# Kernel tuning notes

Hardware: AMD Instinct MI355X
Metric: run time of the kernel (lower is better)

## Reference

```python
import jax, jax.numpy as jnp
import numpy as np

EMBED, HEADS, LEVELS, POINTS, CAMS, ZANCH = 256, 8, 4, 8, 6, 4
HEAD_DIM = EMBED // HEADS
NQ, BS = 10000, 1
SHAPES = np.array([[92, 160], [46, 80], [23, 40], [12, 20]], dtype=np.int64)
NV = int((SHAPES[:, 0] * SHAPES[:, 1]).sum())  # 19560


def setup_inputs() -> dict:
    key = jax.random.key(0)
    ks = jax.random.split(key, 10)
    f = lambda k, s, sc=1.0: jax.random.normal(k, s, dtype=jnp.float32) * sc
    lsi = np.concatenate([[0], np.cumsum(SHAPES[:, 0] * SHAPES[:, 1])[:-1]]).astype(np.int64)
    return dict(
        query=f(ks[0], (BS, NQ, EMBED)),
        query_pos=f(ks[1], (BS, NQ, EMBED)),
        value=f(ks[2], (CAMS, NV, BS, EMBED)),
        reference_points=jax.random.uniform(ks[3], (CAMS, BS, NQ, ZANCH, 2), dtype=jnp.float32),
        bev_mask=jax.random.bernoulli(ks[4], 0.3, (CAMS, BS, NQ, ZANCH)),
        spatial_shapes=jnp.asarray(SHAPES),
        level_start_index=jnp.asarray(lsi),
        Wv=f(ks[5], (EMBED, EMBED), 0.02), bv=jnp.zeros((EMBED,), jnp.float32),
        Woff=f(ks[6], (EMBED, HEADS * LEVELS * POINTS * 2), 0.02),
        boff=f(ks[7], (HEADS * LEVELS * POINTS * 2,), 0.5),
        Watt=f(ks[8], (EMBED, HEADS * LEVELS * POINTS), 0.02),
        batt=jnp.zeros((HEADS * LEVELS * POINTS,), jnp.float32),
        Wout=f(ks[9], (EMBED, EMBED), 0.02), bout=jnp.zeros((EMBED,), jnp.float32),
    )


def _bilinear_gather(v2, x, y, H, W):
    # v2: (BH, H*W, hd); x, y: (BH, N) pixel coords. grid_sample bilinear,
    # align_corners=False, padding_mode='zeros' semantics.
    x0 = jnp.floor(x); y0 = jnp.floor(y)
    lx = x - x0; ly = y - y0
    x0i = x0.astype(jnp.int32); y0i = y0.astype(jnp.int32)
    out = jnp.zeros(x.shape + (v2.shape[-1],), v2.dtype)
    for dx, dy, w in ((0, 0, (1 - lx) * (1 - ly)), (1, 0, lx * (1 - ly)),
                      (0, 1, (1 - lx) * ly), (1, 1, lx * ly)):
        xi = x0i + dx; yi = y0i + dy
        valid = (xi >= 0) & (xi < W) & (yi >= 0) & (yi < H)
        idx = jnp.clip(yi, 0, H - 1) * W + jnp.clip(xi, 0, W - 1)
        g = jnp.take_along_axis(v2, idx[..., None], axis=1)
        out = out + g * (w * valid.astype(v2.dtype))[..., None]
    return out


def _ms_deform_attn(q, v, ref, shapes, lsi, Wv, bv, Woff, boff, Watt, batt):
    # q: (B, nq, C); v: (B, nv, C); ref: (B, nq, D, 2)
    B, nq, C = q.shape
    v = (v @ Wv + bv).reshape(B, -1, HEADS, HEAD_DIM)
    off = (q @ Woff + boff).reshape(B, nq, HEADS, LEVELS, POINTS, 2)
    attw = jax.nn.softmax((q @ Watt + batt).reshape(B, nq, HEADS, LEVELS * POINTS), axis=-1)
    attw = attw.reshape(B, nq, HEADS, LEVELS, POINTS)
    # offset normalizer: (w_l, h_l) per level
    norm = jnp.asarray(np.stack([shapes[:, 1], shapes[:, 0]], -1), q.dtype)  # (L, 2)
    off = off / norm[None, None, None, :, None, :]
    off = off.reshape(B, nq, HEADS, LEVELS, POINTS // ZANCH, ZANCH, 2)
    loc = (ref[:, :, None, None, None] + off).reshape(B, nq, HEADS, LEVELS, POINTS, 2)
    acc = jnp.zeros((B, HEADS, nq, HEAD_DIM), q.dtype)
    for l in range(LEVELS):
        H, W = int(shapes[l, 0]), int(shapes[l, 1])
        s = int(lsi[l])
        vl = v[:, s:s + H * W].transpose(0, 2, 1, 3).reshape(B * HEADS, H * W, HEAD_DIM)
        ll = loc[:, :, :, l].transpose(0, 2, 1, 3, 4).reshape(B * HEADS, nq * POINTS, 2)
        x = ll[..., 0] * W - 0.5
        y = ll[..., 1] * H - 0.5
        samp = _bilinear_gather(vl, x, y, H, W).reshape(B, HEADS, nq, POINTS, HEAD_DIM)
        w = attw[:, :, :, l].transpose(0, 2, 1, 3)  # (B, HEADS, nq, POINTS)
        acc = acc + (samp * w[..., None]).sum(3)
    return acc.transpose(0, 2, 1, 3).reshape(B, nq, C)


def reference(query, query_pos, value, reference_points, bev_mask, spatial_shapes,
              level_start_index, Wv, bv, Woff, boff, Watt, batt, Wout, bout):
    shapes = np.asarray(spatial_shapes)
    lsi = np.asarray(level_start_index)
    B, nq, C = query.shape
    cams = value.shape[0]
    q = query + query_pos
    # replicate queries per camera (equivalent to rebatch-by-mask: unselected
    # outputs are masked out before accumulation)
    q_cam = jnp.broadcast_to(q[:, None], (B, cams, nq, C)).reshape(B * cams, nq, C)
    v = value.transpose(2, 0, 1, 3).reshape(B * cams, -1, C)
    ref = reference_points.transpose(1, 0, 2, 3, 4).reshape(B * cams, nq, ZANCH, 2)
    out = _ms_deform_attn(q_cam, v, ref, shapes, lsi, Wv, bv, Woff, boff, Watt, batt)
    out = out.reshape(B, cams, nq, C)
    # query selection per camera uses batch 0 of bev_mask, as in the original
    m = (bev_mask[:, 0].sum(-1) > 0)  # (cams, nq)
    slots = (out * m[None, :, :, None].astype(out.dtype)).sum(1)  # (B, nq, C)
    count = (bev_mask.sum(-1) > 0).astype(query.dtype).transpose(1, 2, 0).sum(-1)
    count = jnp.maximum(count, 1.0)  # (B, nq)
    slots = slots / count[..., None]
    # dropout in eval mode is identity
    return slots @ Wout + bout + query
```

## Files before the change

### kernel.cpp

```cpp
#include <hip/hip_runtime.h>
#include <hip/hip_bf16.h>

constexpr int NQ = 10000, NV = 19560, CAMS = 6, EMBED = 256, HEADS = 8,
              HEAD_DIM = 32, LEVELS = 4, POINTS = 8;
constexpr int MQ_PAD = 10112;
constexpr int MV_PAD = 117376;

typedef unsigned int u32;
typedef unsigned short u16;
typedef unsigned char u8;
typedef __attribute__((ext_vector_type(8))) short short8v;
typedef __attribute__((ext_vector_type(4))) float f32x4;
typedef __attribute__((ext_vector_type(2))) float f32x2;

__device__ inline u16 f2bf(float f) {
  __hip_bfloat16 b = __float2bfloat16(f);
  return *(u16*)&b;
}

__global__ void conv_bf16_kernel(const float* __restrict__ a, const float* __restrict__ b,
                                 u16* __restrict__ dst, int M, int Mpad) {
  int i = blockIdx.x * blockDim.x + threadIdx.x;
  if (i >= Mpad * 32) return;
  int row = i >> 5;
  int col = (i & 31) * 8;
  u16 o[8];
  if (row < M) {
    const float* pa = a + (size_t)row * 256 + col;
#pragma unroll
    for (int j = 0; j < 8; ++j) {
      float v = pa[j];
      if (b) v += b[(size_t)row * 256 + col + j];
      o[j] = f2bf(v);
    }
  } else {
#pragma unroll
    for (int j = 0; j < 8; ++j) o[j] = 0;
  }
  *(short8v*)&dst[(size_t)row * 256 + col] = *(short8v*)o;
}

__global__ void transpose_w_kernel(const float* __restrict__ src, u16* __restrict__ dst, int N) {
  int g = blockIdx.x * blockDim.x + threadIdx.x;
  if (g >= N * 256) return;
  int n = g >> 8, k = g & 255;
  dst[(size_t)n * 256 + k] = f2bf(src[(size_t)k * N + n]);
}

__global__ void mask_kernel(const int* __restrict__ bev, unsigned char* __restrict__ m,
                            float* __restrict__ cinv) {
  int q = blockIdx.x * blockDim.x + threadIdx.x;
  if (q >= NQ) return;
  int cnt = 0;
  for (int c = 0; c < CAMS; ++c) {
    int any = 0;
    for (int z = 0; z < 4; ++z) any |= bev[((size_t)c * NQ + q) * 4 + z];
    m[c * NQ + q] = (unsigned char)(any != 0);
    cnt += (any != 0);
  }
  cinv[q] = 1.0f / (float)(cnt > 0 ? cnt : 1);
}

__global__ __launch_bounds__(256) void gemm_mfma(
    const u16* __restrict__ A, const u16* __restrict__ Bt,
    const float* __restrict__ bias, const float* __restrict__ add,
    void* __restrict__ Cout, int M, int N, int mode) {
  constexpr int K = 256, BK = 64;
  __shared__ u16 As[128 * BK];
  __shared__ u16 Bs[128 * BK];
  const int tid = threadIdx.x;
  const int lane = tid & 63, w = tid >> 6;
  const int wr = w >> 1, wc = w & 1;
  const int row0 = blockIdx.y * 128, col0 = blockIdx.x * 128;
  f32x4 acc[4][4] = {};

  for (int k0 = 0; k0 < K; k0 += BK) {
    short8v areg[4], breg[4];
#pragma unroll
    for (int j = 0; j < 4; ++j) {
      int e = tid + j * 256;
      int r = e >> 3, cb = (e & 7) * 16;
      areg[j] = *(const short8v*)((const char*)A + ((size_t)(row0 + r) * K + k0) * 2 + cb);
      breg[j] = *(const short8v*)((const char*)Bt + ((size_t)(col0 + r) * K + k0) * 2 + cb);
    }
    __syncthreads();
#pragma unroll
    for (int j = 0; j < 4; ++j) {
      int e = tid + j * 256;
      int r = e >> 3, cb = (e & 7) * 16;
      int sw = cb ^ ((r & 7) << 4);
      *(short8v*)((char*)As + r * 128 + sw) = areg[j];
      *(short8v*)((char*)Bs + r * 128 + sw) = breg[j];
    }
    __syncthreads();
#pragma unroll
    for (int kk = 0; kk < 2; ++kk) {
      short8v af[4], bf[4];
#pragma unroll
      for (int m = 0; m < 4; ++m) {
        int r = wr * 64 + m * 16 + (lane & 15);
        int cb = kk * 64 + (lane >> 4) * 16;
        af[m] = *(const short8v*)((const char*)As + r * 128 + (cb ^ ((r & 7) << 4)));
      }
#pragma unroll
      for (int n = 0; n < 4; ++n) {
        int r = wc * 64 + n * 16 + (lane & 15);
        int cb = kk * 64 + (lane >> 4) * 16;
        bf[n] = *(const short8v*)((const char*)Bs + r * 128 + (cb ^ ((r & 7) << 4)));
      }
#pragma unroll
      for (int m = 0; m < 4; ++m)
#pragma unroll
        for (int n = 0; n < 4; ++n)
          acc[m][n] = __builtin_amdgcn_mfma_f32_16x16x32_bf16(af[m], bf[n], acc[m][n], 0, 0, 0);
    }
  }

#pragma unroll
  for (int m = 0; m < 4; ++m) {
    int rowb = row0 + wr * 64 + m * 16 + (lane >> 4) * 4;
#pragma unroll
    for (int r = 0; r < 4; ++r) {
      int rr = rowb + r;
      if (rr >= M) continue;
#pragma unroll
      for (int n = 0; n < 4; ++n) {
        int col = col0 + wc * 64 + n * 16 + (lane & 15);
        float v = acc[m][n][r] + bias[col];
        if (mode == 0) {
          ((float*)Cout)[(size_t)rr * N + col] = v;
        } else {
          ((float*)Cout)[(size_t)rr * N + col] = v + add[(size_t)rr * N + col];
        }
      }
    }
  }
}

__global__ __launch_bounds__(256) void gemm_wv_f32(
    const float* __restrict__ A, const u16* __restrict__ Bt,
    const float* __restrict__ bias, u8* __restrict__ Cout, int M) {
  constexpr int K = 256, BK = 64, N = 256;
  __shared__ u16 As[128 * BK];
  __shared__ u16 Bs[128 * BK];
  const int tid = threadIdx.x;
  const int lane = tid & 63, w = tid >> 6;
  const int wr = w >> 1, wc = w & 1;
  const int row0 = blockIdx.y * 128, col0 = blockIdx.x * 128;
  f32x4 acc[4][4] = {};

  for (int k0 = 0; k0 < K; k0 += BK) {
    short8v areg[4], breg[4];
#pragma unroll
    for (int j = 0; j < 4; ++j) {
      int e = tid + j * 256;
      int r = e >> 3, co = (e & 7) * 8;
      u16 tmp[8];
      if (row0 + r < M) {
        const float* src = A + (size_t)(row0 + r) * K + k0 + co;
        float4 f0 = *(const float4*)src;
        float4 f1 = *(const float4*)(src + 4);
        tmp[0] = f2bf(f0.x); tmp[1] = f2bf(f0.y); tmp[2] = f2bf(f0.z); tmp[3] = f2bf(f0.w);
        tmp[4] = f2bf(f1.x); tmp[5] = f2bf(f1.y); tmp[6] = f2bf(f1.z); tmp[7] = f2bf(f1.w);
      } else {
#pragma unroll
        for (int t = 0; t < 8; ++t) tmp[t] = 0;
      }
      areg[j] = *(short8v*)tmp;
      breg[j] = *(const short8v*)((const char*)Bt + ((size_t)(col0 + r) * K + k0) * 2 + co * 2);
    }
    __syncthreads();
#pragma unroll
    for (int j = 0; j < 4; ++j) {
      int e = tid + j * 256;
      int r = e >> 3, cb = (e & 7) * 16;
      int sw = cb ^ ((r & 7) << 4);
      *(short8v*)((char*)As + r * 128 + sw) = areg[j];
      *(short8v*)((char*)Bs + r * 128 + sw) = breg[j];
    }
    __syncthreads();
#pragma unroll
    for (int kk = 0; kk < 2; ++kk) {
      short8v af[4], bf[4];
#pragma unroll
      for (int m = 0; m < 4; ++m) {
        int r = wr * 64 + m * 16 + (lane & 15);
        int cb = kk * 64 + (lane >> 4) * 16;
        af[m] = *(const short8v*)((const char*)As + r * 128 + (cb ^ ((r & 7) << 4)));
      }
#pragma unroll
      for (int n = 0; n < 4; ++n) {
        int r = wc * 64 + n * 16 + (lane & 15);
        int cb = kk * 64 + (lane >> 4) * 16;
        bf[n] = *(const short8v*)((const char*)Bs + r * 128 + (cb ^ ((r & 7) << 4)));
      }
#pragma unroll
      for (int m = 0; m < 4; ++m)
#pragma unroll
        for (int n = 0; n < 4; ++n)
          acc[m][n] = __builtin_amdgcn_mfma_f32_16x16x32_bf16(af[m], bf[n], acc[m][n], 0, 0, 0);
    }
  }

#pragma unroll
  for (int m = 0; m < 4; ++m) {
    int rowb = row0 + wr * 64 + m * 16 + (lane >> 4) * 4;
#pragma unroll
    for (int r = 0; r < 4; ++r) {
      int rr = rowb + r;
      if (rr >= M) continue;
      int cam = rr / NV;
      int px = rr - cam * NV;
#pragma unroll
      for (int n = 0; n < 4; ++n) {
        int col = col0 + wc * 64 + n * 16 + (lane & 15);
        float v = acc[m][n][r] + bias[col];
        int h = col >> 5, d = col & 31;
        int pk = __builtin_amdgcn_cvt_pk_fp8_f32(v, v, 0, false);
        Cout[(((size_t)cam * HEADS + h) * NV + px) * 32 + d] = (u8)(pk & 0xff);
      }
    }
  }
}

__global__ void softmax_kernel(float* __restrict__ att) {
  int r = blockIdx.x * blockDim.x + threadIdx.x;
  if (r >= NQ * HEADS) return;
  float* p = att + (size_t)r * 32;
  float mx = -1e30f;
#pragma unroll
  for (int i = 0; i < 32; ++i) mx = fmaxf(mx, p[i]);
  float e[32], sm = 0.f;
#pragma unroll
  for (int i = 0; i < 32; ++i) { e[i] = expf(p[i] - mx); sm += e[i]; }
  float inv = 1.0f / sm;
#pragma unroll
  for (int i = 0; i < 32; ++i) p[i] = e[i] * inv;
}

__global__ __launch_bounds__(256, 8) void sample_kernel(
    const u8* __restrict__ vproj, const float* __restrict__ offr,
    const float* __restrict__ attw, const float* __restrict__ ref,
    const unsigned char* __restrict__ m, float* __restrict__ part) {
  constexpr int Hs[4] = {92, 46, 23, 12};
  constexpr int Ws[4] = {160, 80, 40, 20};
  constexpr int LSI[4] = {0, 14720, 18400, 19320};
  const int c = blockIdx.y;
  const int q = blockIdx.x * 4 + (threadIdx.x >> 6);
  if (!m[c * NQ + q]) return;
  const int lane = threadIdx.x & 63;
  const int h = lane >> 3;
  const int pp = (lane >> 2) & 1;
  const int d0 = (lane & 3) * 8;

  float acc[8] = {};
  const float* refc = ref + ((size_t)c * NQ + q) * 8;
  float rfx[4], rfy[4];
#pragma unroll
  for (int z = 0; z < 4; ++z) { rfx[z] = refc[z * 2]; rfy[z] = refc[z * 2 + 1]; }
  const float* offq = offr + (size_t)q * 512 + h * 64;
  const float* attq = attw + (size_t)q * 256 + h * 32;
  const u8* vch = vproj + ((size_t)c * HEADS + h) * NV * 32 + d0;

#pragma unroll
  for (int l = 0; l < LEVELS; ++l) {
    const int W = Ws[l], H = Hs[l];
    const u8* vl = vch + (size_t)LSI[l] * 32;
#pragma unroll 2
    for (int pi = 0; pi < 4; ++pi) {
      const int p = pi * 2 + pp;
      const int z = p & 3;
      float2 o = *(const float2*)&offq[l * 16 + p * 2];
      float x = rfx[z] * (float)W + o.x - 0.5f;
      float y = rfy[z] * (float)H + o.y - 0.5f;
      float x0f = floorf(x), y0f = floorf(y);
      float lx = x - x0f, ly = y - y0f;
      int x0 = (int)x0f, y0 = (int)y0f;
      float fx0 = (x0 >= 0 && x0 < W) ? 1.f : 0.f;
      float fx1 = (x0 >= -1 && x0 < W - 1) ? 1.f : 0.f;
      float fy0 = (y0 >= 0 && y0 < H) ? 1.f : 0.f;
      float fy1 = (y0 >= -1 && y0 < H - 1) ? 1.f : 0.f;
      int x0c = min(max(x0, 0), W - 1);
      int x1c = min(max(x0 + 1, 0), W - 1);
      int y0c = min(max(y0, 0), H - 1);
      int y1c = min(max(y0 + 1, 0), H - 1);
      uint2 v00 = *(const uint2*)(vl + (size_t)(y0c * W + x0c) * 32);
      uint2 v01 = *(const uint2*)(vl + (size_t)(y0c * W + x1c) * 32);
      uint2 v10 = *(const uint2*)(vl + (size_t)(y1c * W + x0c) * 32);
      uint2 v11 = *(const uint2*)(vl + (size_t)(y1c * W + x1c) * 32);
      float a = attq[l * 8 + p];
      float c00 = a * (1.f - lx) * (1.f - ly) * fx0 * fy0;
      float c01 = a * lx * (1.f - ly) * fx1 * fy0;
      float c10 = a * (1.f - lx) * ly * fx0 * fy1;
      float c11 = a * lx * ly * fx1 * fy1;
#pragma unroll
      for (int half = 0; half < 2; ++half) {
        u32 w00 = half ? v00.y : v00.x, w01 = half ? v01.y : v01.x;
        u32 w10 = half ? v10.y : v10.x, w11 = half ? v11.y : v11.x;
        f32x2 gA0 = __builtin_amdgcn_cvt_pk_f32_fp8(w00, false);
        f32x2 gA1 = __builtin_amdgcn_cvt_pk_f32_fp8(w00, true);
        f32x2 gB0 = __builtin_amdgcn_cvt_pk_f32_fp8(w01, false);
        f32x2 gB1 = __builtin_amdgcn_cvt_pk_f32_fp8(w01, true);
        f32x2 gC0 = __builtin_amdgcn_cvt_pk_f32_fp8(w10, false);
        f32x2 gC1 = __builtin_amdgcn_cvt_pk_f32_fp8(w10, true);
        f32x2 gD0 = __builtin_amdgcn_cvt_pk_f32_fp8(w11, false);
        f32x2 gD1 = __builtin_amdgcn_cvt_pk_f32_fp8(w11, true);
        int b = half * 4;
        acc[b + 0] += c00 * gA0.x + c01 * gB0.x + c10 * gC0.x + c11 * gD0.x;
        acc[b + 1] += c00 * gA0.y + c01 * gB0.y + c10 * gC0.y + c11 * gD0.y;
        acc[b + 2] += c00 * gA1.x + c01 * gB1.x + c10 * gC1.x + c11 * gD1.x;
        acc[b + 3] += c00 * gA1.y + c01 * gB1.y + c10 * gC1.y + c11 * gD1.y;
      }
    }
  }
#pragma unroll
  for (int d = 0; d < 8; ++d) acc[d] += __shfl_xor(acc[d], 4);
  if (pp == 0) {
    float* sp = part + ((size_t)c * NQ + q) * EMBED + h * 32 + d0;
    *(float4*)sp = make_float4(acc[0], acc[1], acc[2], acc[3]);
    *(float4*)(sp + 4) = make_float4(acc[4], acc[5], acc[6], acc[7]);
  }
}

__global__ void reduce_kernel(const float* __restrict__ part, const unsigned char* __restrict__ m,
                              const float* __restrict__ cinv, u16* __restrict__ sbf) {
  int i = blockIdx.x * blockDim.x + threadIdx.x;
  if (i >= MQ_PAD * 32) return;
  int row = i >> 5;
  int col = (i & 31) * 8;
  u16 o[8];
  if (row < NQ) {
    float s[8] = {};
    for (int c = 0; c < CAMS; ++c) {
      if (!m[c * NQ + row]) continue;
      const float* pp = part + ((size_t)c * NQ + row) * EMBED + col;
      float4 f0 = *(const float4*)pp;
      float4 f1 = *(const float4*)(pp + 4);
      s[0] += f0.x; s[1] += f0.y; s[2] += f0.z; s[3] += f0.w;
      s[4] += f1.x; s[5] += f1.y; s[6] += f1.z; s[7] += f1.w;
    }
    float sc = cinv[row];
#pragma unroll
    for (int j = 0; j < 8; ++j) o[j] = f2bf(s[j] * sc);
  } else {
#pragma unroll
    for (int j = 0; j < 8; ++j) o[j] = 0;
  }
  *(short8v*)&sbf[(size_t)row * 256 + col] = *(short8v*)o;
}

extern "C" void kernel_launch(void* const* d_in, const int* in_sizes, int n_in,
                              void* d_out, int out_size, void* d_ws, size_t ws_size,
                              hipStream_t stream) {
  const float* query     = (const float*)d_in[0];
  const float* query_pos = (const float*)d_in[1];
  const float* value     = (const float*)d_in[2];
  const float* refpts    = (const float*)d_in[3];
  const int*   bev       = (const int*)d_in[4];
  const float* Wv   = (const float*)d_in[7];
  const float* bv   = (const float*)d_in[8];
  const float* Woff = (const float*)d_in[9];
  const float* boff = (const float*)d_in[10];
  const float* Watt = (const float*)d_in[11];
  const float* batt = (const float*)d_in[12];
  const float* Wout = (const float*)d_in[13];
  const float* bout = (const float*)d_in[14];
  float* out = (float*)d_out;

  char* ws = (char*)d_ws;
  auto alloc = [&](size_t bytes) {
    char* p = ws;
    ws += (bytes + 255) & ~(size_t)255;
    return p;
  };
  u16*   qbf   = (u16*)alloc((size_t)MQ_PAD * 256 * 2);
  u16*   sbf   = (u16*)alloc((size_t)MQ_PAD * 256 * 2);
  u16*   WvT   = (u16*)alloc((size_t)256 * 256 * 2);
  u16*   WoffT = (u16*)alloc((size_t)512 * 256 * 2);
  u16*   WattT = (u16*)alloc((size_t)256 * 256 * 2);
  u16*   WoutT = (u16*)alloc((size_t)256 * 256 * 2);
  float* offr  = (float*)alloc((size_t)NQ * 512 * 4);
  float* attw  = (float*)alloc((size_t)NQ * 256 * 4);
  u8*    vproj = (u8*)alloc((size_t)CAMS * NV * EMBED);
  float* part  = (float*)alloc((size_t)CAMS * NQ * EMBED * 4);
  float* cinv  = (float*)alloc((size_t)NQ * 4);
  unsigned char* msk = (unsigned char*)alloc((size_t)CAMS * NQ);

  conv_bf16_kernel<<<(MQ_PAD * 32 + 255) / 256, 256, 0, stream>>>(query, query_pos, qbf, NQ, MQ_PAD);
  mask_kernel<<<(NQ + 255) / 256, 256, 0, stream>>>(bev, msk, cinv);
  transpose_w_kernel<<<512, 256, 0, stream>>>(Woff, WoffT, 512);
  transpose_w_kernel<<<256, 256, 0, stream>>>(Watt, WattT, 256);
  transpose_w_kernel<<<256, 256, 0, stream>>>(Wv, WvT, 256);
  transpose_w_kernel<<<256, 256, 0, stream>>>(Wout, WoutT, 256);

  dim3 gOff(512 / 128, MQ_PAD / 128);
  gemm_mfma<<<gOff, 256, 0, stream>>>(qbf, WoffT, boff, nullptr, offr, NQ, 512, 0);
  dim3 gAtt(256 / 128, MQ_PAD / 128);
  gemm_mfma<<<gAtt, 256, 0, stream>>>(qbf, WattT, batt, nullptr, attw, NQ, 256, 0);
  softmax_kernel<<<(NQ * HEADS + 255) / 256, 256, 0, stream>>>(attw);

  dim3 gV(256 / 128, MV_PAD / 128);
  gemm_wv_f32<<<gV, 256, 0, stream>>>(value, WvT, bv, vproj, CAMS * NV);

  dim3 gS(NQ / 4, CAMS);
  sample_kernel<<<gS, 256, 0, stream>>>(vproj, offr, attw, refpts, msk, part);

  reduce_kernel<<<(MQ_PAD * 32 + 255) / 256, 256, 0, stream>>>(part, msk, cinv, sbf);
  gemm_mfma<<<gAtt, 256, 0, stream>>>(sbf, WoutT, bout, query, out, NQ, 256, 2);
}
```

Before: 474.0 us.

## Fuse offset/attention GEMMs, store vproj row-major, and use bf16 partials

Concatenates the offset and attention weight matrices and biases so one GEMM produces both, with softmax and sampling reading from the combined output. The value projection is now stored in plain row-major (cam, pixel, 256) layout instead of head-major, and the point-to-lane assignment in the sampler changes. Per-camera partial sums are written as bf16 instead of fp32, halving reduce traffic at some precision cost. This saves a GEMM launch and memory bandwidth, but gathers now use a 256-byte pixel stride, which may hurt locality across heads.

Result: slower. 901.4 us (+90.2%).

```diff
diff --git a/kernel.cpp b/kernel.cpp
--- a/kernel.cpp
+++ b/kernel.cpp
@@ -17,6 +17,7 @@
   __hip_bfloat16 b = __float2bfloat16(f);
   return *(u16*)&b;
 }
+__device__ inline float bf2f(u16 v) { union { u32 i; float f; } x; x.i = (u32)v << 16; return x.f; }
 
 __global__ void conv_bf16_kernel(const float* __restrict__ a, const float* __restrict__ b,
                                  u16* __restrict__ dst, int M, int Mpad) {
@@ -45,6 +46,13 @@
   if (g >= N * 256) return;
   int n = g >> 8, k = g & 255;
   dst[(size_t)n * 256 + k] = f2bf(src[(size_t)k * N + n]);
+}
+
+__global__ void catbias_kernel(const float* __restrict__ boff, const float* __restrict__ batt,
+                               float* __restrict__ catb) {
+  int i = blockIdx.x * blockDim.x + threadIdx.x;
+  if (i < 512) catb[i] = boff[i];
+  else if (i < 768) catb[i] = batt[i - 512];
 }
 
 __global__ void mask_kernel(const int* __restrict__ bev, unsigned char* __restrict__ m,
@@ -215,18 +223,18 @@
       for (int n = 0; n < 4; ++n) {
         int col = col0 + wc * 64 + n * 16 + (lane & 15);
         float v = acc[m][n][r] + bias[col];
-        int h = col >> 5, d = col & 31;
         int pk = __builtin_amdgcn_cvt_pk_fp8_f32(v, v, 0, false);
-        Cout[(((size_t)cam * HEADS + h) * NV + px) * 32 + d] = (u8)(pk & 0xff);
-      }
-    }
-  }
-}
-
-__global__ void softmax_kernel(float* __restrict__ att) {
+        Cout[((size_t)cam * NV + px) * 256 + col] = (u8)(pk & 0xff);
+      }
+    }
+  }
+}
+
+__global__ void softmax_kernel(float* __restrict__ qout) {
   int r = blockIdx.x * blockDim.x + threadIdx.x;
   if (r >= NQ * HEADS) return;
-  float* p = att + (size_t)r * 32;
+  int q = r >> 3, h = r & 7;
+  float* p = qout + (size_t)q * 768 + 512 + h * 32;
   float mx = -1e30f;
 #pragma unroll
   for (int i = 0; i < 32; ++i) mx = fmaxf(mx, p[i]);
@@ -239,9 +247,9 @@
 }
 
 __global__ __launch_bounds__(256, 8) void sample_kernel(
-    const u8* __restrict__ vproj, const float* __restrict__ offr,
-    const float* __restrict__ attw, const float* __restrict__ ref,
-    const unsigned char* __restrict__ m, float* __restrict__ part) {
+    const u8* __restrict__ vproj, const float* __restrict__ qout,
+    const float* __restrict__ ref, const unsigned char* __restrict__ m,
+    u16* __restrict__ part) {
   constexpr int Hs[4] = {92, 46, 23, 12};
   constexpr int Ws[4] = {160, 80, 40, 20};
   constexpr int LSI[4] = {0, 14720, 18400, 19320};
@@ -258,18 +266,18 @@
   float rfx[4], rfy[4];
 #pragma unroll
   for (int z = 0; z < 4; ++z) { rfx[z] = refc[z * 2]; rfy[z] = refc[z * 2 + 1]; }
-  const float* offq = offr + (size_t)q * 512 + h * 64;
-  const float* attq = attw + (size_t)q * 256 + h * 32;
-  const u8* vch = vproj + ((size_t)c * HEADS + h) * NV * 32 + d0;
+  const float* offq = qout + (size_t)q * 768 + h * 64;
+  const float* attq = qout + (size_t)q * 768 + 512 + h * 32;
+  const u8* vch = vproj + (size_t)c * NV * 256 + h * 32 + d0;
 
 #pragma unroll
   for (int l = 0; l < LEVELS; ++l) {
     const int W = Ws[l], H = Hs[l];
-    const u8* vl = vch + (size_t)LSI[l] * 32;
+    const u8* vl = vch + (size_t)LSI[l] * 256;
 #pragma unroll 2
     for (int pi = 0; pi < 4; ++pi) {
-      const int p = pi * 2 + pp;
-      const int z = p & 3;
+      const int p = pi + 4 * pp;
+      const int z = pi;
       float2 o = *(const float2*)&offq[l * 16 + p * 2];
       float x = rfx[z] * (float)W + o.x - 0.5f;
       float y = rfy[z] * (float)H + o.y - 0.5f;
@@ -284,10 +292,10 @@
       int x1c = min(max(x0 + 1, 0), W - 1);
       int y0c = min(max(y0, 0), H - 1);
       int y1c = min(max(y0 + 1, 0), H - 1);
-      uint2 v00 = *(const uint2*)(vl + (size_t)(y0c * W + x0c) * 32);
-      uint2 v01 = *(const uint2*)(vl + (size_t)(y0c * W + x1c) * 32);
-      uint2 v10 = *(const uint2*)(vl + (size_t)(y1c * W + x0c) * 32);
-      uint2 v11 = *(const uint2*)(vl + (size_t)(y1c * W + x1c) * 32);
+      uint2 v00 = *(const uint2*)(vl + (size_t)(y0c * W + x0c) * 256);
+      uint2 v01 = *(const uint2*)(vl + (size_t)(y0c * W + x1c) * 256);
+      uint2 v10 = *(const uint2*)(vl + (size_t)(y1c * W + x0c) * 256);
+      uint2 v11 = *(const uint2*)(vl + (size_t)(y1c * W + x1c) * 256);
       float a = attq[l * 8 + p];
       float c00 = a * (1.f - lx) * (1.f - ly) * fx0 * fy0;
       float c01 = a * lx * (1.f - ly) * fx1 * fy0;
@@ -316,13 +324,14 @@
 #pragma unroll
   for (int d = 0; d < 8; ++d) acc[d] += __shfl_xor(acc[d], 4);
   if (pp == 0) {
-    float* sp = part + ((size_t)c * NQ + q) * EMBED + h * 32 + d0;
-    *(float4*)sp = make_float4(acc[0], acc[1], acc[2], acc[3]);
-    *(float4*)(sp + 4) = make_float4(acc[4], acc[5], acc[6], acc[7]);
-  }
-}
-
-__global__ void reduce_kernel(const float* __restrict__ part, const unsigned char* __restrict__ m,
+    u16 o[8];
+#pragma unroll
+    for (int d = 0; d < 8; ++d) o[d] = f2bf(acc[d]);
+    *(short8v*)&part[((size_t)c * NQ + q) * EMBED + h * 32 + d0] = *(short8v*)o;
+  }
+}
+
+__global__ void reduce_kernel(const u16* __restrict__ part, const unsigned char* __restrict__ m,
                               const float* __restrict__ cinv, u16* __restrict__ sbf) {
   int i = blockIdx.x * blockDim.x + threadIdx.x;
   if (i >= MQ_PAD * 32) return;
@@ -333,11 +342,9 @@
     float s[8] = {};
     for (int c = 0; c < CAMS; ++c) {
       if (!m[c * NQ + row]) continue;
-      const float* pp = part + ((size_t)c * NQ + row) * EMBED + col;
-      float4 f0 = *(const float4*)pp;
-      float4 f1 = *(const float4*)(pp + 4);
-      s[0] += f0.x; s[1] += f0.y; s[2] += f0.z; s[3] += f0.w;
-      s[4] += f1.x; s[5] += f1.y; s[6] += f1.z; s[7] += f1.w;
+      short8v v = *(const short8v*)&part[((size_t)c * NQ + row) * EMBED + col];
+#pragma unroll
+      for (int j = 0; j < 8; ++j) s[j] += bf2f((u16)v[j]);
     }
     float sc = cinv[row];
 #pragma unroll
@@ -376,35 +383,34 @@
   u16*   qbf   = (u16*)alloc((size_t)MQ_PAD * 256 * 2);
   u16*   sbf   = (u16*)alloc((size_t)MQ_PAD * 256 * 2);
   u16*   WvT   = (u16*)alloc((size_t)256 * 256 * 2);
-  u16*   WoffT = (u16*)alloc((size_t)512 * 256 * 2);
-  u16*   WattT = (u16*)alloc((size_t)256 * 256 * 2);
+  u16*   WqT   = (u16*)alloc((size_t)768 * 256 * 2);
   u16*   WoutT = (u16*)alloc((size_t)256 * 256 * 2);
-  float* offr  = (float*)alloc((size_t)NQ * 512 * 4);
-  float* attw  = (float*)alloc((size_t)NQ * 256 * 4);
+  float* catb  = (float*)alloc((size_t)768 * 4);
+  float* qout  = (float*)alloc((size_t)MQ_PAD * 768 * 4);
   u8*    vproj = (u8*)alloc((size_t)CAMS * NV * EMBED);
-  float* part  = (float*)alloc((size_t)CAMS * NQ * EMBED * 4);
+  u16*   part  = (u16*)alloc((size_t)CAMS * NQ * EMBED * 2);
   float* cinv  = (float*)alloc((size_t)NQ * 4);
   unsigned char* msk = (unsigned char*)alloc((size_t)CAMS * NQ);
 
   conv_bf16_kernel<<<(MQ_PAD * 32 + 255) / 256, 256, 0, stream>>>(query, query_pos, qbf, NQ, MQ_PAD);
   mask_kernel<<<(NQ + 255) / 256, 256, 0, stream>>>(bev, msk, cinv);
-  transpose_w_kernel<<<512, 256, 0, stream>>>(Woff, WoffT, 512);
-  transpose_w_kernel<<<256, 256, 0, stream>>>(Watt, WattT, 256);
+  transpose_w_kernel<<<512, 256, 0, stream>>>(Woff, WqT, 512);
+  transpose_w_kernel<<<256, 256, 0, stream>>>(Watt, WqT + (size_t)512 * 256, 256);
   transpose_w_kernel<<<256, 256, 0, stream>>>(Wv, WvT, 256);
   transpose_w_kernel<<<256, 256, 0, stream>>>(Wout, WoutT, 256);
-
-  dim3 gOff(512 / 128, MQ_PAD / 128);
-  gemm_mfma<<<gOff, 256, 0, stream>>>(qbf, WoffT, boff, nullptr, offr, NQ, 512, 0);
-  dim3 gAtt(256 / 128, MQ_PAD / 128);
-  gemm_mfma<<<gAtt, 256, 0, stream>>>(qbf, WattT, batt, nullptr, attw, NQ, 256, 0);
-  softmax_kernel<<<(NQ * HEADS + 255) / 256, 256, 0, stream>>>(attw);
+  catbias_kernel<<<3, 256, 0, stream>>>(boff, batt, catb);
+
+  dim3 gQ(768 / 128, MQ_PAD / 128);
+  gemm_mfma<<<gQ, 256, 0, stream>>>(qbf, WqT, catb, nullptr, qout, NQ, 768, 0);
+  softmax_kernel<<<(NQ * HEADS + 255) / 256, 256, 0, stream>>>(qout);
 
   dim3 gV(256 / 128, MV_PAD / 128);
   gemm_wv_f32<<<gV, 256, 0, stream>>>(value, WvT, bv, vproj, CAMS * NV);
 
   dim3 gS(NQ / 4, CAMS);
-  sample_kernel<<<gS, 256, 0, stream>>>(vproj, offr, attw, refpts, msk, part);
+  sample_kernel<<<gS, 256, 0, stream>>>(vproj, qout, refpts, msk, part);
 
   reduce_kernel<<<(MQ_PAD * 32 + 255) / 256, 256, 0, stream>>>(part, msk, cinv, sbf);
-  gemm_mfma<<<gAtt, 256, 0, stream>>>(sbf, WoutT, bout, query, out, NQ, 256, 2);
-}
+  dim3 gOut(256 / 128, MQ_PAD / 128);
+  gemm_mfma<<<gOut, 256, 0, stream>>>(sbf, WoutT, bout, query, out, NQ, 256, 2);
+}
```
